# Kernel optimization log

Measured on AMD Instinct MI355X. Metric: run time of the kernel, lower is better.

## Reference

```python
import jax, jax.numpy as jnp
import numpy as np

NUM_HEADS = 16
TOP_K = 2

def setup_inputs() -> dict:
    key = jax.random.key(0)
    ks = jax.random.split(key, 5)
    B, D, E = 8192, 2048, 8
    x = jax.random.normal(ks[0], (B, D), dtype=jnp.float32)
    W_qkv = jax.random.normal(ks[1], (E, D, 3 * D), dtype=jnp.float32) * 0.02  # (in,out) per expert
    W_gate = jax.random.normal(ks[2], (D, E), dtype=jnp.float32) * 0.02
    b_gate = jnp.zeros((E,), dtype=jnp.float32)
    W_proj = jax.random.normal(ks[3], (D, D), dtype=jnp.float32) * 0.02
    b_proj = jnp.zeros((D,), dtype=jnp.float32)
    return {"x": x, "W_qkv": W_qkv, "W_gate": W_gate, "b_gate": b_gate,
            "W_proj": W_proj, "b_proj": b_proj}


def reference(x, W_qkv, W_gate, b_gate, W_proj, b_proj):
    B, D = x.shape
    E = W_qkv.shape[0]
    H = NUM_HEADS
    hd = D // H
    scale = float(hd) ** -0.5

    # gating + top-k (sparse gate weights, zeros for non-selected experts)
    gate_scores = jax.nn.softmax(x @ W_gate + b_gate, axis=-1)        # (B, E)
    topk_vals, topk_idx = jax.lax.top_k(gate_scores, TOP_K)           # (B, K)
    gw = jnp.zeros_like(gate_scores).at[jnp.arange(B)[:, None], topk_idx].add(topk_vals)

    # gate-weighted combine of expert QKV projections (linear => combine after GEMM)
    qkv = jnp.zeros((B, 3 * D), dtype=x.dtype)
    for e in range(E):  # fixed small expert count; each iter is one big GEMM
        qkv = qkv + gw[:, e:e + 1] * (x @ W_qkv[e])
    qkv = qkv.reshape(B, 3, H, hd)

    # NOTE: the torch source writes `q = k = v = torch.zeros(...)` then uses
    # in-place `+=`, so q, k, v ALIAS one tensor: all equal gate*(q_i+k_i+v_i).
    # We replicate that exact math faithfully.
    s = qkv.sum(axis=1)                                               # (B, H, hd)

    attn = jax.nn.softmax(jnp.einsum('bhd,bgd->bhg', s, s) * scale, axis=-1)  # (B, H, H)
    out = jnp.einsum('bhg,bgd->bhd', attn, s)                         # (B, H, hd)
    out = out.transpose(0, 2, 1).reshape(B, D)                        # matches .transpose(1,2).reshape
    return out @ W_proj + b_proj
```

## Files before the change

kernel.cpp:

```cpp
#include <hip/hip_runtime.h>

#define B_ROWS 8192
#define DDIM 2048
#define NEXP 8
#define NASSIGN (B_ROWS * 2)
#define MAX_TILES 80
#define KBLK 131072

typedef unsigned short u16;
typedef short bf16x8 __attribute__((ext_vector_type(8)));
typedef float f32x4 __attribute__((ext_vector_type(4)));

#define M_CNT 0
#define M_FILL 8
#define M_SEG 16
#define M_TE 32
#define M_TB 112
#define M_TR 192

__device__ __forceinline__ u16 f2b(float f) {
  union { float f; unsigned u; } c; c.f = f;
  return (u16)((c.u + 0x7fffu + ((c.u >> 16) & 1u)) >> 16);
}
__device__ __forceinline__ float b2f(u16 h) {
  union { unsigned u; float f; } c; c.u = ((unsigned)h) << 16;
  return c.f;
}
__device__ __forceinline__ void async16(u16* lds, const u16* g) {
  __builtin_amdgcn_global_load_lds(
      (const __attribute__((address_space(1))) unsigned int*)g,
      (__attribute__((address_space(3))) unsigned int*)lds, 16, 0, 0);
}

__global__ void init_meta_kernel(int* meta) {
  int t = threadIdx.x;
  if (t < 32) meta[t] = 0;
}

__global__ __launch_bounds__(256) void prologue_kernel(
    const float* __restrict__ x, const float* __restrict__ Wqkv,
    const float* __restrict__ Wg, const float* __restrict__ bg,
    const float* __restrict__ Wp, u16* __restrict__ xb,
    u16* __restrict__ WsumT, u16* __restrict__ WprojT,
    int* __restrict__ e01, float* __restrict__ w01, int* __restrict__ meta) {
  __shared__ __align__(16) float ldsF[3][64][64];
  __shared__ double red[4][8];
  const int orig = blockIdx.x;
  const int bid = (orig & 7) * 2176 + (orig >> 3);
  const int t = threadIdx.x;

  if (bid < 9216) {
    const float* Win;
    u16* Wout;
    int ldin, nsum, bx;
    if (bid < 8192) { Win = Wqkv; Wout = WsumT; ldin = 3 * DDIM; nsum = 3; bx = bid; }
    else            { Win = Wp;   Wout = WprojT; ldin = DDIM;    nsum = 1; bx = bid - 8192; }
    int nt = bx & 31, kt = (bx >> 5) & 31, e = bx >> 10;
    const size_t in_base = (size_t)e * DDIM * (size_t)ldin;
    int k0 = kt * 64, n0 = nt * 64;
    for (int ci = 0; ci < nsum; ++ci) {
#pragma unroll
      for (int i = 0; i < 4; ++i) {
        int idx = i * 256 + t;
        int kl = idx >> 4, f4 = idx & 15;
        const float* p =
            Win + in_base + (size_t)(k0 + kl) * ldin + ci * 2048 + n0 + f4 * 4;
        async16((u16*)&ldsF[ci][kl][f4 * 4], (const u16*)p);
      }
    }
    __syncthreads();
    u16* out = Wout + ((size_t)e * 32 + kt) * KBLK;
    {
      int n = t >> 2, kc = t & 3;
      u16 r[16];
#pragma unroll
      for (int j = 0; j < 16; ++j) {
        int k = kc * 16 + j;
        float v = ldsF[0][k][n];
        if (nsum == 3) v += ldsF[1][k][n] + ldsF[2][k][n];
        r[j] = f2b(v);
      }
      uint4 pk0, pk1;
      pk0.x = (unsigned)r[0] | ((unsigned)r[1] << 16);
      pk0.y = (unsigned)r[2] | ((unsigned)r[3] << 16);
      pk0.z = (unsigned)r[4] | ((unsigned)r[5] << 16);
      pk0.w = (unsigned)r[6] | ((unsigned)r[7] << 16);
      pk1.x = (unsigned)r[8] | ((unsigned)r[9] << 16);
      pk1.y = (unsigned)r[10] | ((unsigned)r[11] << 16);
      pk1.z = (unsigned)r[12] | ((unsigned)r[13] << 16);
      pk1.w = (unsigned)r[14] | ((unsigned)r[15] << 16);
      u16* op = out + (size_t)(n0 + n) * 64 + kc * 16;
      *(uint4*)op = pk0;
      *(uint4*)(op + 8) = pk1;
    }
    return;
  }

  const int b = bid - 9216;
  const float* xr = x + (size_t)b * DDIM;
  float4 v0 = ((const float4*)xr)[2 * t];
  float4 v1 = ((const float4*)xr)[2 * t + 1];
  float xv[8] = {v0.x, v0.y, v0.z, v0.w, v1.x, v1.y, v1.z, v1.w};
  uint4 pk;
  pk.x = (unsigned)f2b(xv[0]) | ((unsigned)f2b(xv[1]) << 16);
  pk.y = (unsigned)f2b(xv[2]) | ((unsigned)f2b(xv[3]) << 16);
  pk.z = (unsigned)f2b(xv[4]) | ((unsigned)f2b(xv[5]) << 16);
  pk.w = (unsigned)f2b(xv[6]) | ((unsigned)f2b(xv[7]) << 16);
  *(uint4*)(xb + (size_t)b * DDIM + t * 8) = pk;

  double acc[8] = {0, 0, 0, 0, 0, 0, 0, 0};
#pragma unroll
  for (int j = 0; j < 8; ++j) {
    const float4* wr = (const float4*)(Wg + (size_t)(t * 8 + j) * 8);
    float4 wa = wr[0], wb = wr[1];
    double xd = (double)xv[j];
    acc[0] += xd * wa.x; acc[1] += xd * wa.y;
    acc[2] += xd * wa.z; acc[3] += xd * wa.w;
    acc[4] += xd * wb.x; acc[5] += xd * wb.y;
    acc[6] += xd * wb.z; acc[7] += xd * wb.w;
  }
#pragma unroll
  for (int e = 0; e < 8; ++e)
    for (int m2 = 32; m2; m2 >>= 1) acc[e] += __shfl_xor(acc[e], m2);
  if ((t & 63) == 0)
    for (int e = 0; e < 8; ++e) red[t >> 6][e] = acc[e];
  __syncthreads();
  if (t == 0) {
    double l[8];
    for (int e = 0; e < 8; ++e)
      l[e] = red[0][e] + red[1][e] + red[2][e] + red[3][e] + (double)bg[e];
    double mx = l[0];
    for (int e = 1; e < 8; ++e) mx = l[e] > mx ? l[e] : mx;
    double p[8], s = 0;
    for (int e = 0; e < 8; ++e) { p[e] = exp(l[e] - mx); s += p[e]; }
    int i1 = 0;
    for (int e = 1; e < 8; ++e) if (p[e] > p[i1]) i1 = e;
    int i2 = (i1 == 0) ? 1 : 0;
    for (int e = 0; e < 8; ++e)
      if (e != i1 && p[e] > p[i2]) i2 = e;
    e01[2 * b] = i1; e01[2 * b + 1] = i2;
    w01[2 * b] = (float)(p[i1] / s);
    w01[2 * b + 1] = (float)(p[i2] / s);
    atomicAdd(&meta[M_CNT + i1], 1);
    atomicAdd(&meta[M_CNT + i2], 1);
  }
}

__global__ __launch_bounds__(128) void scan_kernel(int* meta) {
  __shared__ int scnt[8];
  int t = threadIdx.x;
  if (t < 8) scnt[t] = meta[M_CNT + t];
  __syncthreads();
  int seg[9], pre[9];
  seg[0] = 0; pre[0] = 0;
#pragma unroll
  for (int e = 0; e < 8; ++e) {
    seg[e + 1] = seg[e] + scnt[e];
    pre[e + 1] = pre[e] + ((scnt[e] + 255) >> 8);
  }
  if (t < 8) meta[M_SEG + t] = seg[t];
  if (t < MAX_TILES) {
    if (t < pre[8]) {
      int e = 0;
      while (e < 7 && t >= pre[e + 1]) ++e;
      int i = t - pre[e];
      meta[M_TE + t] = e;
      meta[M_TB + t] = seg[e] + i * 256;
      meta[M_TR + t] = scnt[e] - i * 256;
    } else {
      meta[M_TE + t] = 0; meta[M_TB + t] = 0; meta[M_TR + t] = 0;
    }
  }
}

__global__ __launch_bounds__(256) void build_kernel(
    const int* __restrict__ e01, const float* __restrict__ w01,
    int* __restrict__ meta, int* __restrict__ rows, float* __restrict__ wt,
    int* __restrict__ rowpos) {
  int b = blockIdx.x * 256 + threadIdx.x;
  if (b >= B_ROWS) return;
#pragma unroll
  for (int s = 0; s < 2; ++s) {
    int e = e01[2 * b + s];
    float w = w01[2 * b + s];
    int p = meta[M_SEG + e] + atomicAdd(&meta[M_FILL + e], 1);
    rows[p] = b;
    wt[p] = w;
    rowpos[2 * b + s] = p;
  }
}

#define BAR()                           \
  do {                                  \
    __builtin_amdgcn_sched_barrier(0);  \
    __builtin_amdgcn_s_barrier();       \
    __builtin_amdgcn_sched_barrier(0);  \
  } while (0)
#define VMCNT2() asm volatile("s_waitcnt vmcnt(2)" ::: "memory")
#define VMCNT0() asm volatile("s_waitcnt vmcnt(0)" ::: "memory")
#define LGKM0()                                       \
  do {                                                \
    asm volatile("s_waitcnt lgkmcnt(0)" ::: "memory"); \
    __builtin_amdgcn_sched_barrier(0);                \
  } while (0)

#define STAGE_A(L, T, BB) async16(&lds[BB][0][(L)*4096 + t * 8], srcA[L] + (size_t)(T)*64)
#define STAGE_B(L, T, BB) async16(&lds[BB][1][(L)*4096 + t * 8], srcB[L] + (size_t)(T)*KBLK)

#define READ_A(QM)                                                   \
  do {                                                               \
    _Pragma("unroll") for (int i_ = 0; i_ < 4; ++i_) {               \
      int rb_ = baseA + ((QM)*64 + i_ * 16) * 128;                   \
      af[i_][0] = *(const bf16x8*)(pA + rb_ + ck0);                  \
      af[i_][1] = *(const bf16x8*)(pA + rb_ + ck1);                  \
    }                                                                \
  } while (0)
#define READ_B(H)                                                    \
  do {                                                               \
    _Pragma("unroll") for (int j_ = 0; j_ < 2; ++j_) {               \
      int rb_ = baseB + (((H)*2 + j_) * 16) * 128;                   \
      bfr[(H)*2 + j_][0] = *(const bf16x8*)(pB + rb_ + ck0);         \
      bfr[(H)*2 + j_][1] = *(const bf16x8*)(pB + rb_ + ck1);         \
    }                                                                \
  } while (0)
#define MFMA16(QM, QN)                                                         \
  do {                                                                         \
    _Pragma("unroll") for (int i_ = 0; i_ < 4; ++i_) {                         \
      _Pragma("unroll") for (int j_ = 0; j_ < 2; ++j_) {                       \
        acc[(QM)*4 + i_][(QN)*2 + j_] = __builtin_amdgcn_mfma_f32_16x16x32_bf16( \
            af[i_][0], bfr[(QN)*2 + j_][0], acc[(QM)*4 + i_][(QN)*2 + j_], 0, 0, 0); \
        acc[(QM)*4 + i_][(QN)*2 + j_] = __builtin_amdgcn_mfma_f32_16x16x32_bf16( \
            af[i_][1], bfr[(QN)*2 + j_][1], acc[(QM)*4 + i_][(QN)*2 + j_], 0, 0, 0); \
      }                                                                        \
    }                                                                          \
  } while (0)

template <int MODE>
__global__ __launch_bounds__(512, 2) void gemm256_kernel(
    const u16* __restrict__ A, const u16* __restrict__ BT,
    const int* __restrict__ meta, const int* __restrict__ rows,
    const float* __restrict__ wt, const float* __restrict__ bias,
    u16* __restrict__ Yc, float* __restrict__ Out) {
  __shared__ __align__(16) u16 lds[2][2][16384];

  int e = 0, base = 0, rem = 256, m0 = 0;
  if (MODE == 0) {
    rem = meta[M_TR + blockIdx.y];
    if (rem <= 0) return;
    if (rem > 256) rem = 256;
    e = meta[M_TE + blockIdx.y];
    base = meta[M_TB + blockIdx.y];
  } else {
    m0 = blockIdx.y * 256;
  }
  const int n0 = blockIdx.x * 256;
  const int t = threadIdx.x;
  const int lane = t & 63;
  const int wid = t >> 6;
  const int wr = wid >> 2, wc = wid & 3;
  const int l15 = lane & 15;
  const int kg = lane >> 4;
  const int sw = lane & 7;

  const u16* srcA[4];
  const u16* srcB[4];
#pragma unroll
  for (int L = 0; L < 4; ++L) {
    int row = L * 64 + (t >> 3);
    int cl = (t & 7) ^ (row & 7);
    int grow;
    if (MODE == 0) {
      int rl = row < rem ? row : 0;
      grow = rows[base + rl];
    } else {
      grow = m0 + row;
    }
    srcA[L] = A + (size_t)grow * DDIM + cl * 8;
    srcB[L] = BT + (size_t)e * DDIM * DDIM + (size_t)(n0 + row) * 64 + cl * 8;
  }

  f32x4 acc[8][4];
#pragma unroll
  for (int i = 0; i < 8; ++i)
#pragma unroll
    for (int j = 0; j < 4; ++j) {
      f32x4 z = {0.f, 0.f, 0.f, 0.f};
      acc[i][j] = z;
    }

  const int baseA = (wr * 128 + l15) * 128;
  const int baseB = (wc * 64 + l15) * 128;
  const int ck0 = ((0 * 4 + kg) ^ sw) << 4;
  const int ck1 = ((1 * 4 + kg) ^ sw) << 4;

  bf16x8 af[4][2];
  bf16x8 bfr[4][2];

  STAGE_A(0, 0, 0); STAGE_A(1, 0, 0); STAGE_A(2, 0, 0); STAGE_A(3, 0, 0);
  STAGE_B(0, 0, 0); STAGE_B(1, 0, 0); STAGE_B(2, 0, 0); STAGE_B(3, 0, 0);
  STAGE_A(0, 1, 1); STAGE_A(1, 1, 1);
  VMCNT2();
  BAR();

  const int NT = DDIM / 64;
  for (int T = 0; T < NT; ++T) {
    const int cb = T & 1, nb = cb ^ 1;
    const char* pA = (const char*)&lds[cb][0][0];
    const char* pB = (const char*)&lds[cb][1][0];
    READ_A(0);
    READ_B(0);
    if (T + 1 < NT) { STAGE_A(2, T + 1, nb); STAGE_A(3, T + 1, nb); }
    BAR();
    LGKM0();
    __builtin_amdgcn_s_setprio(1);
    MFMA16(0, 0);
    __builtin_amdgcn_s_setprio(0);
    BAR();
    READ_B(1);
    if (T + 1 < NT) { STAGE_B(0, T + 1, nb); STAGE_B(1, T + 1, nb); }
    BAR();
    LGKM0();
    __builtin_amdgcn_s_setprio(1);
    MFMA16(0, 1);
    __builtin_amdgcn_s_setprio(0);
    BAR();
    READ_A(1);
    if (T + 1 < NT) { STAGE_B(2, T + 1, nb); STAGE_B(3, T + 1, nb); }
    BAR();
    LGKM0();
    __builtin_amdgcn_s_setprio(1);
    MFMA16(1, 0);
    __builtin_amdgcn_s_setprio(0);
    BAR();
    if (T + 2 < NT) {
      STAGE_A(0, T + 2, cb); STAGE_A(1, T + 2, cb);
      VMCNT2();
    } else {
      VMCNT0();
    }
    BAR();
    __builtin_amdgcn_s_setprio(1);
    MFMA16(1, 1);
    __builtin_amdgcn_s_setprio(0);
    BAR();
  }

  if (MODE == 1) {
    float bv[4];
#pragma unroll
    for (int fn = 0; fn < 4; ++fn) bv[fn] = bias[n0 + wc * 64 + fn * 16 + l15];
#pragma unroll
    for (int qm = 0; qm < 2; ++qm)
#pragma unroll
      for (int i = 0; i < 4; ++i)
#pragma unroll
        for (int r = 0; r < 4; ++r) {
          int rl = wr * 128 + qm * 64 + i * 16 + kg * 4 + r;
          float* orow = Out + (size_t)(m0 + rl) * DDIM + n0 + wc * 64 + l15;
#pragma unroll
          for (int fn = 0; fn < 4; ++fn)
            orow[fn * 16] = acc[qm * 4 + i][fn][r] + bv[fn];
        }
  } else {
#pragma unroll
    for (int qm = 0; qm < 2; ++qm)
#pragma unroll
      for (int i = 0; i < 4; ++i)
#pragma unroll
        for (int r = 0; r < 4; ++r) {
          int rl = wr * 128 + qm * 64 + i * 16 + kg * 4 + r;
          if (rl < rem) {
            int pos = base + rl;
            float w = wt[pos];
            u16* yrow = Yc + (size_t)pos * DDIM + n0 + wc * 64 + l15;
#pragma unroll
            for (int fn = 0; fn < 4; ++fn)
              yrow[fn * 16] = f2b(w * acc[qm * 4 + i][fn][r]);
          }
        }
  }
}

__global__ __launch_bounds__(64) void combine_attn_kernel(
    const u16* __restrict__ Yc, const int* __restrict__ rowpos,
    u16* __restrict__ ab) {
  __shared__ __align__(16) u16 sb[16][136];
  __shared__ __align__(16) u16 pl[16][20];
  const int b = blockIdx.x, l = threadIdx.x;
  const int p0 = rowpos[2 * b], p1 = rowpos[2 * b + 1];
  const uint4* r0 = (const uint4*)(Yc + (size_t)p0 * DDIM + l * 32);
  const uint4* r1 = (const uint4*)(Yc + (size_t)p1 * DDIM + l * 32);
  {
    const int h = l >> 2, cbase = (l & 3) * 32;
#pragma unroll
    for (int q = 0; q < 4; ++q) {
      uint4 a = r0[q], c = r1[q];
      const unsigned* au = (const unsigned*)&a;
      const unsigned* cu = (const unsigned*)&c;
      uint4 w;
      unsigned* wu = (unsigned*)&w;
#pragma unroll
      for (int j = 0; j < 4; ++j) {
        float lo = b2f((u16)(au[j] & 0xffff)) + b2f((u16)(cu[j] & 0xffff));
        float hi = b2f((u16)(au[j] >> 16)) + b2f((u16)(cu[j] >> 16));
        wu[j] = (unsigned)f2b(lo) | ((unsigned)f2b(hi) << 16);
      }
      *(uint4*)&sb[h][cbase + q * 8] = w;
    }
  }
  __syncthreads();
  const int hh = l & 15, kg = l >> 4;
  f32x4 S = {0.f, 0.f, 0.f, 0.f};
#pragma unroll
  for (int kc = 0; kc < 4; ++kc) {
    bf16x8 f = *(const bf16x8*)&sb[hh][kc * 32 + kg * 8];
    S = __builtin_amdgcn_mfma_f32_16x16x32_bf16(f, f, S, 0, 0, 0);
  }
  const float sc = 0.088388347648318447f;
  float lg[4];
  float mx = -1e30f;
#pragma unroll
  for (int r = 0; r < 4; ++r) { lg[r] = S[r] * sc; mx = fmaxf(mx, lg[r]); }
  mx = fmaxf(mx, __shfl_xor(mx, 16));
  mx = fmaxf(mx, __shfl_xor(mx, 32));
  float p[4], sum = 0.f;
#pragma unroll
  for (int r = 0; r < 4; ++r) { p[r] = expf(lg[r] - mx); sum += p[r]; }
  sum += __shfl_xor(sum, 16);
  sum += __shfl_xor(sum, 32);
  const float inv = 1.f / sum;
#pragma unroll
  for (int r = 0; r < 4; ++r) pl[hh][kg * 4 + r] = f2b(p[r] * inv);
  __syncthreads();
  bf16x8 pa = {0, 0, 0, 0, 0, 0, 0, 0};
  if (kg < 2) pa = *(const bf16x8*)&pl[hh][kg * 8];
  u16* orow = ab + (size_t)b * DDIM;
#pragma unroll
  for (int c = 0; c < 8; ++c) {
    bf16x8 bv = {0, 0, 0, 0, 0, 0, 0, 0};
    if (kg < 2) {
      u16* bvp = (u16*)&bv;
#pragma unroll
      for (int j = 0; j < 8; ++j) bvp[j] = sb[kg * 8 + j][c * 16 + hh];
    }
    f32x4 z = {0.f, 0.f, 0.f, 0.f};
    f32x4 o = __builtin_amdgcn_mfma_f32_16x16x32_bf16(pa, bv, z, 0, 0, 0);
    uint2 st;
    st.x = (unsigned)f2b(o[0]) | ((unsigned)f2b(o[1]) << 16);
    st.y = (unsigned)f2b(o[2]) | ((unsigned)f2b(o[3]) << 16);
    *(uint2*)(orow + (c * 16 + hh) * 16 + kg * 4) = st;
  }
}

extern "C" void kernel_launch(void* const* d_in, const int* in_sizes, int n_in,
                              void* d_out, int out_size, void* d_ws, size_t ws_size,
                              hipStream_t stream) {
  const float* x = (const float*)d_in[0];
  const float* Wqkv = (const float*)d_in[1];
  const float* Wg = (const float*)d_in[2];
  const float* bg = (const float*)d_in[3];
  const float* Wp = (const float*)d_in[4];
  const float* bp = (const float*)d_in[5];
  float* out = (float*)d_out;

  char* ws = (char*)d_ws;
  size_t off = 0;
  auto alloc = [&](size_t bytes) {
    void* p = ws + off;
    off += (bytes + 255) & ~(size_t)255;
    return p;
  };
  u16* xb = (u16*)alloc((size_t)B_ROWS * DDIM * 2);
  u16* WsumT = (u16*)alloc((size_t)NEXP * DDIM * DDIM * 2);
  u16* WprojT = (u16*)alloc((size_t)DDIM * DDIM * 2);
  u16* Yc = (u16*)alloc((size_t)NASSIGN * DDIM * 2);
  u16* ab = (u16*)alloc((size_t)B_ROWS * DDIM * 2);
  int* e01 = (int*)alloc((size_t)NASSIGN * 4);
  float* w01 = (float*)alloc((size_t)NASSIGN * 4);
  int* rows = (int*)alloc((size_t)NASSIGN * 4);
  float* wt = (float*)alloc((size_t)NASSIGN * 4);
  int* rowpos = (int*)alloc((size_t)NASSIGN * 4);
  int* meta = (int*)alloc(4096);

  init_meta_kernel<<<dim3(1), dim3(64), 0, stream>>>(meta);
  prologue_kernel<<<dim3(17408), dim3(256), 0, stream>>>(
      x, Wqkv, Wg, bg, Wp, xb, WsumT, WprojT, e01, w01, meta);
  scan_kernel<<<dim3(1), dim3(128), 0, stream>>>(meta);
  build_kernel<<<dim3(32), dim3(256), 0, stream>>>(e01, w01, meta, rows, wt, rowpos);
  gemm256_kernel<0><<<dim3(8, MAX_TILES), dim3(512), 0, stream>>>(
      xb, WsumT, meta, rows, wt, nullptr, Yc, nullptr);
  combine_attn_kernel<<<dim3(B_ROWS), dim3(64), 0, stream>>>(Yc, rowpos, ab);
  gemm256_kernel<1><<<dim3(8, 32), dim3(512), 0, stream>>>(
      ab, WprojT, meta, rows, wt, bp, nullptr, out);
  (void)in_sizes; (void)n_in; (void)out_size; (void)ws_size;
}
```

Before: 587.9 us.

## Split expert QKV weight sum/transpose into row-streaming panel kernel

```diff
diff --git a/kernel.cpp b/kernel.cpp
--- a/kernel.cpp
+++ b/kernel.cpp
@@ -37,49 +37,82 @@
   if (t < 32) meta[t] = 0;
 }
 
+__global__ __launch_bounds__(256) void prep_rows_kernel(
+    const float* __restrict__ Wqkv, u16* __restrict__ WsumT) {
+  __shared__ u16 panel[2048][36];
+  const int bid = blockIdx.x;
+  const int e = bid >> 5, kt = bid & 31;
+  const int t = threadIdx.x;
+  const float* rowbase = Wqkv + (size_t)e * 2048 * 6144 + (size_t)kt * 64 * 6144;
+  u16* out = WsumT + ((size_t)e * 32 + kt) * KBLK;
+
+  for (int half = 0; half < 2; ++half) {
+#pragma unroll 4
+    for (int kk = 0; kk < 32; ++kk) {
+      const float* row = rowbase + (size_t)(half * 32 + kk) * 6144;
+      float4 a0 = *(const float4*)(row + t * 8);
+      float4 a1 = *(const float4*)(row + t * 8 + 4);
+      float4 b0 = *(const float4*)(row + 2048 + t * 8);
+      float4 b1 = *(const float4*)(row + 2048 + t * 8 + 4);
+      float4 c0 = *(const float4*)(row + 4096 + t * 8);
+      float4 c1 = *(const float4*)(row + 4096 + t * 8 + 4);
+      u16 r[8];
+      r[0] = f2b(a0.x + b0.x + c0.x); r[1] = f2b(a0.y + b0.y + c0.y);
+      r[2] = f2b(a0.z + b0.z + c0.z); r[3] = f2b(a0.w + b0.w + c0.w);
+      r[4] = f2b(a1.x + b1.x + c1.x); r[5] = f2b(a1.y + b1.y + c1.y);
+      r[6] = f2b(a1.z + b1.z + c1.z); r[7] = f2b(a1.w + b1.w + c1.w);
+#pragma unroll
+      for (int j = 0; j < 8; ++j) panel[t * 8 + j][kk] = r[j];
+    }
+    __syncthreads();
+#pragma unroll
+    for (int i = 0; i < 8; ++i) {
+      int n = t + 256 * i;
+      const uint2* pr = (const uint2*)&panel[n][0];
+      uint2 q0 = pr[0], q1 = pr[1], q2 = pr[2], q3 = pr[3];
+      uint2 q4 = pr[4], q5 = pr[5], q6 = pr[6], q7 = pr[7];
+      u16* op = out + (size_t)n * 64 + half * 32;
+      uint4 w0 = {q0.x, q0.y, q1.x, q1.y};
+      uint4 w1 = {q2.x, q2.y, q3.x, q3.y};
+      uint4 w2 = {q4.x, q4.y, q5.x, q5.y};
+      uint4 w3 = {q6.x, q6.y, q7.x, q7.y};
+      *(uint4*)op = w0;
+      *(uint4*)(op + 8) = w1;
+      *(uint4*)(op + 16) = w2;
+      *(uint4*)(op + 24) = w3;
+    }
+    __syncthreads();
+  }
+}
+
 __global__ __launch_bounds__(256) void prologue_kernel(
-    const float* __restrict__ x, const float* __restrict__ Wqkv,
-    const float* __restrict__ Wg, const float* __restrict__ bg,
-    const float* __restrict__ Wp, u16* __restrict__ xb,
-    u16* __restrict__ WsumT, u16* __restrict__ WprojT,
+    const float* __restrict__ x, const float* __restrict__ Wg,
+    const float* __restrict__ bg, const float* __restrict__ Wp,
+    u16* __restrict__ xb, u16* __restrict__ WprojT,
     int* __restrict__ e01, float* __restrict__ w01, int* __restrict__ meta) {
-  __shared__ __align__(16) float ldsF[3][64][64];
+  __shared__ __align__(16) float ldsF[64][64];
   __shared__ double red[4][8];
-  const int orig = blockIdx.x;
-  const int bid = (orig & 7) * 2176 + (orig >> 3);
+  const int bid = 8192 + blockIdx.x;
   const int t = threadIdx.x;
 
   if (bid < 9216) {
-    const float* Win;
-    u16* Wout;
-    int ldin, nsum, bx;
-    if (bid < 8192) { Win = Wqkv; Wout = WsumT; ldin = 3 * DDIM; nsum = 3; bx = bid; }
-    else            { Win = Wp;   Wout = WprojT; ldin = DDIM;    nsum = 1; bx = bid - 8192; }
-    int nt = bx & 31, kt = (bx >> 5) & 31, e = bx >> 10;
-    const size_t in_base = (size_t)e * DDIM * (size_t)ldin;
+    int bx = bid - 8192;
+    int nt = bx & 31, kt = (bx >> 5) & 31;
     int k0 = kt * 64, n0 = nt * 64;
-    for (int ci = 0; ci < nsum; ++ci) {
-#pragma unroll
-      for (int i = 0; i < 4; ++i) {
-        int idx = i * 256 + t;
-        int kl = idx >> 4, f4 = idx & 15;
-        const float* p =
-            Win + in_base + (size_t)(k0 + kl) * ldin + ci * 2048 + n0 + f4 * 4;
-        async16((u16*)&ldsF[ci][kl][f4 * 4], (const u16*)p);
-      }
+#pragma unroll
+    for (int i = 0; i < 4; ++i) {
+      int idx = i * 256 + t;
+      int kl = idx >> 4, f4 = idx & 15;
+      const float* p = Wp + (size_t)(k0 + kl) * DDIM + n0 + f4 * 4;
+      async16((u16*)&ldsF[kl][f4 * 4], (const u16*)p);
     }
     __syncthreads();
-    u16* out = Wout + ((size_t)e * 32 + kt) * KBLK;
+    u16* out = WprojT + (size_t)kt * KBLK;
     {
       int n = t >> 2, kc = t & 3;
       u16 r[16];
 #pragma unroll
-      for (int j = 0; j < 16; ++j) {
-        int k = kc * 16 + j;
-        float v = ldsF[0][k][n];
-        if (nsum == 3) v += ldsF[1][k][n] + ldsF[2][k][n];
-        r[j] = f2b(v);
-      }
+      for (int j = 0; j < 16; ++j) r[j] = f2b(ldsF[kc * 16 + j][n]);
       uint4 pk0, pk1;
       pk0.x = (unsigned)r[0] | ((unsigned)r[1] << 16);
       pk0.y = (unsigned)r[2] | ((unsigned)r[3] << 16);
@@ -483,8 +516,9 @@
   int* meta = (int*)alloc(4096);
 
   init_meta_kernel<<<dim3(1), dim3(64), 0, stream>>>(meta);
-  prologue_kernel<<<dim3(17408), dim3(256), 0, stream>>>(
-      x, Wqkv, Wg, bg, Wp, xb, WsumT, WprojT, e01, w01, meta);
+  prep_rows_kernel<<<dim3(256), dim3(256), 0, stream>>>(Wqkv, WsumT);
+  prologue_kernel<<<dim3(9216), dim3(256), 0, stream>>>(
+      x, Wg, bg, Wp, xb, WprojT, e01, w01, meta);
   scan_kernel<<<dim3(1), dim3(128), 0, stream>>>(meta);
   build_kernel<<<dim3(32), dim3(256), 0, stream>>>(e01, w01, meta, rows, wt, rowpos);
   gemm256_kernel<0><<<dim3(8, MAX_TILES), dim3(512), 0, stream>>>(
```

Measured after the change: 683.5 us. 16.3% more time.
